# Performance work log

Hardware: AMD Instinct MI355X
Metric: run time of the kernel (lower is better)

The kernel has to match this reference:

```python
import jax, jax.numpy as jnp
import numpy as np

B, N, D = 4, 2048, 4
COUPLING = 1.0
DT = 1.0


def setup_inputs() -> dict:
    key = jax.random.key(0)
    k1, k2, k3, k4 = jax.random.split(key, 4)
    theta_prev = jax.random.normal(k1, (B, N, D), dtype=jnp.float32)
    gamma_t = jax.random.normal(k2, (B, N, D), dtype=jnp.float32)
    affinity = jax.random.uniform(k3, (B, N, N), dtype=jnp.float32)
    alpha_t = jax.random.normal(k4, (B, N, N), dtype=jnp.float32)
    # learned parameters, initialized as in the torch module
    omega = jnp.zeros((N, D), dtype=jnp.float32)
    kappa = jnp.ones((N, D), dtype=jnp.float32)
    alpha_bias = jnp.zeros((N, N), dtype=jnp.float32)
    return {
        "theta_prev": theta_prev,
        "gamma_t": gamma_t,
        "affinity": affinity,
        "alpha_t": alpha_t,
        "omega": omega,
        "kappa": kappa,
        "alpha_bias": alpha_bias,
    }


def reference(theta_prev, gamma_t, affinity, alpha_t, omega, kappa, alpha_bias):
    # theta_prev: [B, N, D], affinity/alpha_t: [B, N, N]
    n = theta_prev.shape[1]
    alpha_total = alpha_t + alpha_bias[None, :, :]               # [B, N, N]
    # phase_term[b, i, j, d] = sin(theta[b, j, d] - theta[b, i, d] - alpha_total[b, i, j])
    phase_term = jnp.sin(
        theta_prev[:, None, :, :] - theta_prev[:, :, None, :]
        - alpha_total[:, :, :, None]
    )                                                            # [B, N, N, D]
    coupling_term = (COUPLING / n) * jnp.einsum(
        "bij,bijd->bid", affinity, phase_term
    )                                                            # [B, N, D]
    drive_term = kappa[None, :, :] * (gamma_t - theta_prev)
    theta_dot = omega[None, :, :] + drive_term + coupling_term
    return theta_prev + DT * theta_dot
```

## Files before the change

kernel.cpp:

```cpp
#include <hip/hip_runtime.h>

#define BB 4
#define NN 2048
#define DD 4
#define ROWS 4
#define BLOCK 256

__global__ __launch_bounds__(BLOCK) void sincos_theta(const float* __restrict__ theta,
                                                      float* __restrict__ sArr,
                                                      float* __restrict__ cArr) {
    const int idx = blockIdx.x * BLOCK + threadIdx.x;
    const float x = theta[idx];
    float s, c;
    __sincosf(x, &s, &c);
    sArr[idx] = s;
    cArr[idx] = c;
}

__global__ __launch_bounds__(BLOCK) void kuramoto_main(
    const float* __restrict__ theta,
    const float* __restrict__ gam,
    const float* __restrict__ aff,
    const float* __restrict__ alp,
    const float* __restrict__ omega,
    const float* __restrict__ kappa,
    const float* __restrict__ bias,
    const float* __restrict__ sArr,
    const float* __restrict__ cArr,
    float* __restrict__ out)
{
    const int tid = threadIdx.x;
    const int blk = blockIdx.x;
    const int rowBlocks = NN / ROWS;
    const int b  = blk / rowBlocks;
    const int i0 = (blk % rowBlocks) * ROWS;

    const float* __restrict__ aff_b = aff + (size_t)b * NN * NN;
    const float* __restrict__ alp_b = alp + (size_t)b * NN * NN;
    const float4* __restrict__ s4 = (const float4*)sArr + (size_t)b * NN;
    const float4* __restrict__ c4 = (const float4*)cArr + (size_t)b * NN;

    float accU[ROWS][DD];
    float accV[ROWS][DD];
    #pragma unroll
    for (int r = 0; r < ROWS; ++r)
        #pragma unroll
        for (int d = 0; d < DD; ++d) { accU[r][d] = 0.f; accV[r][d] = 0.f; }

    for (int jj = 0; jj < NN / BLOCK; ++jj) {
        const int j = tid + jj * BLOCK;
        const float4 sj = s4[j];
        const float4 cj = c4[j];
        #pragma unroll
        for (int r = 0; r < ROWS; ++r) {
            const size_t off = (size_t)(i0 + r) * NN + j;
            const float a  = aff_b[off];
            const float al = alp_b[off] + bias[off];
            float sa, ca;
            __sincosf(al, &sa, &ca);
            const float wc = a * ca;
            const float ws = a * sa;
            accU[r][0] = fmaf(wc, sj.x, fmaf(-ws, cj.x, accU[r][0]));
            accU[r][1] = fmaf(wc, sj.y, fmaf(-ws, cj.y, accU[r][1]));
            accU[r][2] = fmaf(wc, sj.z, fmaf(-ws, cj.z, accU[r][2]));
            accU[r][3] = fmaf(wc, sj.w, fmaf(-ws, cj.w, accU[r][3]));
            accV[r][0] = fmaf(wc, cj.x, fmaf(ws, sj.x, accV[r][0]));
            accV[r][1] = fmaf(wc, cj.y, fmaf(ws, sj.y, accV[r][1]));
            accV[r][2] = fmaf(wc, cj.z, fmaf(ws, sj.z, accV[r][2]));
            accV[r][3] = fmaf(wc, cj.w, fmaf(ws, sj.w, accV[r][3]));
        }
    }

    __shared__ float red[BLOCK / 64][ROWS * 2 * DD];
    const int wave = tid >> 6;
    const int lane = tid & 63;

    #pragma unroll
    for (int r = 0; r < ROWS; ++r) {
        #pragma unroll
        for (int d = 0; d < DD; ++d) {
            float u = accU[r][d];
            float v = accV[r][d];
            #pragma unroll
            for (int off = 32; off >= 1; off >>= 1) {
                u += __shfl_down(u, off, 64);
                v += __shfl_down(v, off, 64);
            }
            if (lane == 0) {
                red[wave][r * 2 * DD + d]      = u;
                red[wave][r * 2 * DD + DD + d] = v;
            }
        }
    }
    __syncthreads();

    if (tid < ROWS * DD) {
        const int r = tid >> 2;
        const int d = tid & 3;
        float U = 0.f, V = 0.f;
        #pragma unroll
        for (int w = 0; w < BLOCK / 64; ++w) {
            U += red[w][r * 2 * DD + d];
            V += red[w][r * 2 * DD + DD + d];
        }
        const int i = i0 + r;
        const int idx = (b * NN + i) * DD + d;
        const float s_i = sArr[idx];
        const float c_i = cArr[idx];
        const float coup = (1.0f / (float)NN) * (c_i * U - s_i * V);
        const float th = theta[idx];
        const float o  = omega[i * DD + d];
        const float k  = kappa[i * DD + d];
        out[idx] = th + o + k * (gam[idx] - th) + coup;
    }
}

extern "C" void kernel_launch(void* const* d_in, const int* in_sizes, int n_in,
                              void* d_out, int out_size, void* d_ws, size_t ws_size,
                              hipStream_t stream) {
    const float* theta = (const float*)d_in[0];
    const float* gam   = (const float*)d_in[1];
    const float* aff   = (const float*)d_in[2];
    const float* alp   = (const float*)d_in[3];
    const float* omega = (const float*)d_in[4];
    const float* kappa = (const float*)d_in[5];
    const float* bias  = (const float*)d_in[6];
    float* out  = (float*)d_out;

    float* sArr = (float*)d_ws;
    float* cArr = sArr + BB * NN * DD;

    sincos_theta<<<(BB * NN * DD) / BLOCK, BLOCK, 0, stream>>>(theta, sArr, cArr);
    kuramoto_main<<<(BB * NN) / ROWS, BLOCK, 0, stream>>>(
        theta, gam, aff, alp, omega, kappa, bias, sArr, cArr, out);
}
```

Baseline: 178.7 us.

## Vectorize row loads to float4 with nontemporal hints and halve rows per block

Each thread now handles four consecutive columns per step, loading affinity, alpha and bias as 16-byte vectors, with nontemporal hints on the two large streamed matrices. Rows per block drop from four to two, doubling the grid to add more blocks in flight. The j loop is fully unrolled. The aim is to raise memory-level parallelism and cut load instruction count on this bandwidth-bound kernel, at the cost of more register pressure and more reloads of the per-batch sin/cos vectors across blocks.

```diff
diff --git a/kernel.cpp b/kernel.cpp
--- a/kernel.cpp
+++ b/kernel.cpp
@@ -3,8 +3,12 @@
 #define BB 4
 #define NN 2048
 #define DD 4
-#define ROWS 4
+#define ROWS 2
 #define BLOCK 256
+#define QPT 4
+#define JITER (NN / (BLOCK * QPT))
+
+typedef float f4 __attribute__((ext_vector_type(4)));
 
 __global__ __launch_bounds__(BLOCK) void sincos_theta(const float* __restrict__ theta,
                                                       float* __restrict__ sArr,
@@ -35,10 +39,11 @@
     const int b  = blk / rowBlocks;
     const int i0 = (blk % rowBlocks) * ROWS;
 
-    const float* __restrict__ aff_b = aff + (size_t)b * NN * NN;
-    const float* __restrict__ alp_b = alp + (size_t)b * NN * NN;
-    const float4* __restrict__ s4 = (const float4*)sArr + (size_t)b * NN;
-    const float4* __restrict__ c4 = (const float4*)cArr + (size_t)b * NN;
+    const f4* __restrict__ aff4 = (const f4*)(aff + (size_t)b * NN * NN);
+    const f4* __restrict__ alp4 = (const f4*)(alp + (size_t)b * NN * NN);
+    const f4* __restrict__ bia4 = (const f4*)bias;
+    const f4* __restrict__ s4   = (const f4*)sArr + (size_t)b * NN;
+    const f4* __restrict__ c4   = (const f4*)cArr + (size_t)b * NN;
 
     float accU[ROWS][DD];
     float accV[ROWS][DD];
@@ -47,27 +52,43 @@
         #pragma unroll
         for (int d = 0; d < DD; ++d) { accU[r][d] = 0.f; accV[r][d] = 0.f; }
 
-    for (int jj = 0; jj < NN / BLOCK; ++jj) {
-        const int j = tid + jj * BLOCK;
-        const float4 sj = s4[j];
-        const float4 cj = c4[j];
+    #pragma unroll
+    for (int jj = 0; jj < JITER; ++jj) {
+        const int q  = jj * BLOCK + tid;
+        const int j0 = q * QPT;
+
+        f4 av[ROWS], lv[ROWS], bv[ROWS];
         #pragma unroll
         for (int r = 0; r < ROWS; ++r) {
-            const size_t off = (size_t)(i0 + r) * NN + j;
-            const float a  = aff_b[off];
-            const float al = alp_b[off] + bias[off];
-            float sa, ca;
-            __sincosf(al, &sa, &ca);
-            const float wc = a * ca;
-            const float ws = a * sa;
-            accU[r][0] = fmaf(wc, sj.x, fmaf(-ws, cj.x, accU[r][0]));
-            accU[r][1] = fmaf(wc, sj.y, fmaf(-ws, cj.y, accU[r][1]));
-            accU[r][2] = fmaf(wc, sj.z, fmaf(-ws, cj.z, accU[r][2]));
-            accU[r][3] = fmaf(wc, sj.w, fmaf(-ws, cj.w, accU[r][3]));
-            accV[r][0] = fmaf(wc, cj.x, fmaf(ws, sj.x, accV[r][0]));
-            accV[r][1] = fmaf(wc, cj.y, fmaf(ws, sj.y, accV[r][1]));
-            accV[r][2] = fmaf(wc, cj.z, fmaf(ws, sj.z, accV[r][2]));
-            accV[r][3] = fmaf(wc, cj.w, fmaf(ws, sj.w, accV[r][3]));
+            const size_t qo = (size_t)(i0 + r) * (NN / QPT) + q;
+            av[r] = __builtin_nontemporal_load(&aff4[qo]);
+            lv[r] = __builtin_nontemporal_load(&alp4[qo]);
+            bv[r] = bia4[qo];
+        }
+        f4 sj[QPT], cj[QPT];
+        #pragma unroll
+        for (int u = 0; u < QPT; ++u) { sj[u] = s4[j0 + u]; cj[u] = c4[j0 + u]; }
+
+        #pragma unroll
+        for (int r = 0; r < ROWS; ++r) {
+            const f4 alr = lv[r] + bv[r];
+            const float aA[4] = {av[r].x, av[r].y, av[r].z, av[r].w};
+            const float lA[4] = {alr.x, alr.y, alr.z, alr.w};
+            #pragma unroll
+            for (int u = 0; u < QPT; ++u) {
+                float sa, ca;
+                __sincosf(lA[u], &sa, &ca);
+                const float wc = aA[u] * ca;
+                const float ws = aA[u] * sa;
+                accU[r][0] = fmaf(wc, sj[u].x, fmaf(-ws, cj[u].x, accU[r][0]));
+                accU[r][1] = fmaf(wc, sj[u].y, fmaf(-ws, cj[u].y, accU[r][1]));
+                accU[r][2] = fmaf(wc, sj[u].z, fmaf(-ws, cj[u].z, accU[r][2]));
+                accU[r][3] = fmaf(wc, sj[u].w, fmaf(-ws, cj[u].w, accU[r][3]));
+                accV[r][0] = fmaf(wc, cj[u].x, fmaf(ws, sj[u].x, accV[r][0]));
+                accV[r][1] = fmaf(wc, cj[u].y, fmaf(ws, sj[u].y, accV[r][1]));
+                accV[r][2] = fmaf(wc, cj[u].z, fmaf(ws, sj[u].z, accV[r][2]));
+                accV[r][3] = fmaf(wc, cj[u].w, fmaf(ws, sj[u].w, accV[r][3]));
+            }
         }
     }
 
```

After: 178.2 us. No clear change (-0.3%).
